# Kernel optimization log

Measured on AMD Instinct MI355X. Metric: run time of the kernel, lower is better.

Reference implementation:

```python
import jax, jax.numpy as jnp
import numpy as np

B, DP, N = 8, 3, 2048
DM, K = 128, 20
C4 = DM // 4


def _gather(pts, idx):
    # pts: (b, n, c), idx: (b, n, k) -> (b, n, k, c)
    return jax.vmap(lambda p, i: p[i])(pts, idx)


def _bn(x, gamma, beta, eps=1e-5):
    # train-mode BatchNorm1d; x: (b, c, n), stats over (batch, points)
    mu = jnp.mean(x, axis=(0, 2), keepdims=True)
    var = jnp.var(x, axis=(0, 2), keepdims=True)
    return gamma[None, :, None] * (x - mu) * jax.lax.rsqrt(var + eps) + beta[None, :, None]


def setup_inputs() -> dict:
    key = jax.random.key(0)
    ks = iter(jax.random.split(key, 32))

    def U(shape):
        s = 1.0 / np.sqrt(shape[-1])
        return jax.random.uniform(next(ks), shape, jnp.float32, -s, s)

    d = {}
    d['features'] = jax.random.normal(next(ks), (B, DP, N), jnp.float32)
    d['fc1_w'] = U((DM, DP)); d['fc1_b'] = U((DM,))
    d['fc2_w'] = U((DM, DM)); d['fc2_b'] = U((DM,))
    d['bn_g'] = jnp.ones((DM,), jnp.float32); d['bn_b'] = jnp.zeros((DM,), jnp.float32)
    d['fb1_w'] = U((DM, 2 * DP)); d['fb1_b'] = U((DM,))
    d['fb2_w'] = U((DM, DM)); d['fb2_b'] = U((DM,))
    d['fg1_w'] = U((DM, DM)); d['fg1_b'] = U((DM,))
    d['fg2_w'] = U((DM, DM)); d['fg2_b'] = U((DM,))
    d['wq'] = U((DM, DM)); d['wk'] = U((DM, DM)); d['wv'] = U((DM, DM))
    d['sa_qk_w'] = U((C4, DM))  # q_conv and k_conv share this weight
    d['sa_v_w'] = U((DM, DM)); d['sa_v_b'] = U((DM,))
    d['sa_t_w'] = U((DM, DM)); d['sa_t_b'] = U((DM,))
    d['sa_bn_g'] = jnp.ones((DM,), jnp.float32); d['sa_bn_b'] = jnp.zeros((DM,), jnp.float32)
    return d


def reference(features, fc1_w, fc1_b, fc2_w, fc2_b, bn_g, bn_b,
              fb1_w, fb1_b, fb2_w, fb2_b, fg1_w, fg1_b, fg2_w, fg2_b,
              wq, wk, wv, sa_qk_w, sa_v_w, sa_v_b, sa_t_w, sa_t_b,
              sa_bn_g, sa_bn_b):
    x = features  # (b, dp, n)
    # --- kNN: negative squared pairwise distance, top-k largest = nearest ---
    inner = -2.0 * jnp.einsum('bdn,bdm->bnm', x, x)
    xx = jnp.sum(x * x, axis=1)  # (b, n)
    pd = -xx[:, :, None] - inner - xx[:, None, :]  # (b, n, n)
    idx = jax.lax.top_k(pd, K)[1]  # (b, n, K) neighbor indices
    # --- get_graph_feature: gather neighbors, concat (nbr - ctr, ctr) ---
    xt = jnp.transpose(x, (0, 2, 1))  # (b, n, dp)
    nbr = _gather(xt, idx)  # (b, n, K, dp)
    ctr = jnp.broadcast_to(xt[:, :, None, :], nbr.shape)
    kf = jnp.concatenate([nbr - ctr, ctr], axis=-1)  # (b, n, K, 2*dp)
    # fb edge MLP
    kf = jax.nn.relu(kf @ fb1_w.T + fb1_b) @ fb2_w.T + fb2_b  # (b, n, K, DM)
    # --- point-transformer attention ---
    x1 = xt @ fc1_w.T + fc1_b  # (b, n, DM)
    q = x1 @ wq.T
    kg = _gather(x1 @ wk.T, idx)  # (b, n, K, DM)
    vg = _gather(x1 @ wv.T, idx)  # (b, n, K, DM)
    a = q[:, :, None, :] - kg + kf
    a = jax.nn.relu(a @ fg1_w.T + fg1_b) @ fg2_w.T + fg2_b  # fc_gamma
    attn = jax.nn.log_softmax(a / jnp.sqrt(jnp.float32(DM)), axis=-2)  # over K
    res = jnp.einsum('bnkf,bnkf->bnf', attn, vg + kf)  # (b, n, DM)
    res = jnp.transpose(res @ fc2_w.T + fc2_b, (0, 2, 1))  # (b, DM, n)
    res = jax.nn.relu(_bn(res, bn_g, bn_b)) + jnp.transpose(x1, (0, 2, 1))
    # --- SA_Layer: offset self-attention (q and k share weights) ---
    xqk = jnp.einsum('cd,bdn->bcn', sa_qk_w, res)  # (b, C4, n)
    energy = jnp.einsum('bcn,bcm->bnm', xqk, xqk)  # (b, n, n)
    att = jax.nn.softmax(energy, axis=-1)
    att = att / (1e-9 + jnp.sum(att, axis=1, keepdims=True))
    xv = jnp.einsum('cd,bdn->bcn', sa_v_w, res) + sa_v_b[None, :, None]
    xr = jnp.einsum('bcn,bnm->bcm', xv, att)  # x_v @ attention
    xr = jnp.einsum('cd,bdn->bcn', sa_t_w, res - xr) + sa_t_b[None, :, None]
    xr = jax.nn.relu(_bn(xr, sa_bn_g, sa_bn_b))
    out = res + xr  # (b, DM, n)
    return (jnp.transpose(out, (0, 2, 1)), attn)
```

## Files before the change

### kernel.cpp

```cpp
#include <hip/hip_runtime.h>

#define NPTS 16384
#define NB 2048
#define KNN 20

typedef __attribute__((ext_vector_type(4))) float f32x4;
typedef __attribute__((ext_vector_type(8))) short short8;

union U4S8 { uint4 q; short8 s; };
union W4   { unsigned u[4]; short8 s; };

__device__ __forceinline__ unsigned bf16_rne(float v){
    unsigned u = __float_as_uint(v);
    return (u + 0x7fffu + ((u>>16)&1u)) >> 16;
}
__device__ __forceinline__ unsigned pack_hl(float v){
    unsigned hi = bf16_rne(v);
    float r = v - __uint_as_float(hi<<16);
    unsigned lo = bf16_rne(r);
    return hi | (lo<<16);
}
__device__ __forceinline__ void split_hl(uint4 w0, uint4 w1, short8& hi, short8& lo){
    W4 h, l;
    h.u[0] = __builtin_amdgcn_perm(w0.y, w0.x, 0x05040100u);
    l.u[0] = __builtin_amdgcn_perm(w0.y, w0.x, 0x07060302u);
    h.u[1] = __builtin_amdgcn_perm(w0.w, w0.z, 0x05040100u);
    l.u[1] = __builtin_amdgcn_perm(w0.w, w0.z, 0x07060302u);
    h.u[2] = __builtin_amdgcn_perm(w1.y, w1.x, 0x05040100u);
    l.u[2] = __builtin_amdgcn_perm(w1.y, w1.x, 0x07060302u);
    h.u[3] = __builtin_amdgcn_perm(w1.w, w1.z, 0x05040100u);
    l.u[3] = __builtin_amdgcn_perm(w1.w, w1.z, 0x07060302u);
    hi = h.s; lo = l.s;
}
__device__ __forceinline__ f32x4 e3_mfma(short8 Ah, short8 Al, short8 Bh, short8 Bl){
    f32x4 acc = (f32x4){0.f,0.f,0.f,0.f};
    acc = __builtin_amdgcn_mfma_f32_16x16x32_bf16(Al, Bh, acc, 0,0,0);
    acc = __builtin_amdgcn_mfma_f32_16x16x32_bf16(Ah, Bl, acc, 0,0,0);
    acc = __builtin_amdgcn_mfma_f32_16x16x32_bf16(Ah, Bh, acc, 0,0,0);
    return acc;
}

__global__ void transpose_kernel(const float* in, float* out, int C){
    int gid = blockIdx.x*256 + threadIdx.x;
    if (gid >= 128*C) return;
    int j = gid / C, c = gid - j*C;
    out[gid] = in[c*128 + j];
}

__global__ void pack_bfrag_kernel(const float* w0, const float* w1, const float* w2, unsigned short* out){
    int gid = blockIdx.x*256 + threadIdx.x;
    if (gid >= 3*16384) return;
    int m = gid >> 14, r = gid & 16383;
    const float* W = (m==0)?w0:(m==1)?w1:w2;
    int e = r & 7, lane = (r>>3) & 63, ks = (r>>9)&3, ct = r>>11;
    int c = ct*16 + (lane&15), j = ks*32 + (lane>>4)*8 + e;
    out[gid] = (unsigned short)bf16_rne(W[c*128 + j]);
}

__global__ __launch_bounds__(256) void knn_kernel(const float* feat, int* g_idx){
    __shared__ float sx[2048], sy[2048], sz[2048];
    __shared__ int swin[32*20];
    int tid = threadIdx.x;
    int p0 = blockIdx.x * 32;
    int b = p0 >> 11;
    const float* fb = feat + b*3*2048;
    for (int i = tid; i < 2048; i += 256){ sx[i]=fb[i]; sy[i]=fb[2048+i]; sz[i]=fb[4096+i]; }
    __syncthreads();

    int chunk = tid & 7, pl = tid >> 3;
    int n = (p0 + pl) & 2047;
    double xi = sx[n], yi = sy[n], zi = sz[n];

    const double SENT = __longlong_as_double(0x7FE0000000000000ll);
    double val[20];
#pragma unroll
    for (int k=0;k<20;k++) val[k] = SENT;

    int base = chunk*256;
    for (int ii=0; ii<256; ii++){
        int i = (ii + (chunk<<2)) & 255;
        int j = base + i;
        double dx = (double)sx[j]-xi, dy = (double)sy[j]-yi, dz = (double)sz[j]-zi;
        double d2 = dx*dx + dy*dy + dz*dz;
        long long kb = ((__double_as_longlong(d2) & ~2047ll) | (long long)j) + (1ll<<61);
        double key = __longlong_as_double(kb);
#pragma unroll
        for (int s=19; s>=1; s--)
            val[s] = fmax(val[s-1], fmin(val[s], key));
        val[0] = fmin(val[0], key);
    }

    for (int kk=0; kk<20; kk++){
        double h = val[0];
        h = fmin(h, __shfl_xor(h, 1));
        h = fmin(h, __shfl_xor(h, 2));
        h = fmin(h, __shfl_xor(h, 4));
        if (val[0] == h){
            swin[pl*20 + kk] = (int)(__double_as_longlong(h) & 2047ll);
#pragma unroll
            for (int s=0;s<19;s++) val[s] = val[s+1];
            val[19] = SENT;
        }
    }
    __syncthreads();
    for (int t = tid; t < 640; t += 256)
        g_idx[p0*20 + t] = swin[t];
}

__global__ void x1_kernel(const float* feat, const float* w, const float* bias, float* x1){
    int gid = blockIdx.x*256 + threadIdx.x;
    int p = gid >> 7, c = gid & 127;
    int b = p >> 11, n = p & 2047;
    const float* fb = feat + b*6144 + n;
    float v = bias[c];
    v += w[c*3+0]*fb[0];
    v += w[c*3+1]*fb[2048];
    v += w[c*3+2]*fb[4096];
    x1[gid] = v;
}

__global__ __launch_bounds__(256) void qkv_kernel(const float* x1, const float* wqT, const float* wkT,
                                                  const float* wvT, float* q, float* k1, float* v1){
    __shared__ float sx[16][128];
    int tid = threadIdx.x;
    int p0 = blockIdx.x * 16;
    for (int t = tid; t < 2048; t += 256) sx[t>>7][t&127] = x1[p0*128 + t];
    __syncthreads();
    int cg = tid & 31, pg = tid >> 5, c0 = cg*4;
    float aq[2][4] = {{0,0,0,0},{0,0,0,0}};
    float ak[2][4] = {{0,0,0,0},{0,0,0,0}};
    float av[2][4] = {{0,0,0,0},{0,0,0,0}};
    for (int j=0;j<128;j++){
        float xa = sx[pg][j], xb = sx[pg+8][j];
        float4 wq4 = *(const float4*)&wqT[j*128 + c0];
        float4 wk4 = *(const float4*)&wkT[j*128 + c0];
        float4 wv4 = *(const float4*)&wvT[j*128 + c0];
        const float* wqp = &wq4.x; const float* wkp = &wk4.x; const float* wvp = &wv4.x;
#pragma unroll
        for (int ci=0; ci<4; ci++){
            aq[0][ci] += wqp[ci]*xa; aq[1][ci] += wqp[ci]*xb;
            ak[0][ci] += wkp[ci]*xa; ak[1][ci] += wkp[ci]*xb;
            av[0][ci] += wvp[ci]*xa; av[1][ci] += wvp[ci]*xb;
        }
    }
#pragma unroll
    for (int pp=0; pp<2; pp++){
        int p = p0 + pg + pp*8;
        *(float4*)&q [p*128 + c0] = make_float4(aq[pp][0],aq[pp][1],aq[pp][2],aq[pp][3]);
        *(float4*)&k1[p*128 + c0] = make_float4(ak[pp][0],ak[pp][1],ak[pp][2],ak[pp][3]);
        *(float4*)&v1[p*128 + c0] = make_float4(av[pp][0],av[pp][1],av[pp][2],av[pp][3]);
    }
}

__device__ __forceinline__ void stage_gemm(const unsigned* buf, const unsigned short* wb,
                                           int lane, int ct0, f32x4 acc[5][2]){
    short8 bf[2][4];
#pragma unroll
    for (int ci=0; ci<2; ci++)
#pragma unroll
    for (int ks=0; ks<4; ks++){
        U4S8 u; u.q = *(const uint4*)(wb + ((ct0+ci)*4 + ks)*512 + lane*8);
        bf[ci][ks] = u.s;
    }
#pragma unroll
    for (int rt=0; rt<5; rt++)
#pragma unroll
    for (int ci=0; ci<2; ci++)
        acc[rt][ci] = (f32x4){0.f,0.f,0.f,0.f};
    int abase = (lane&15)*132 + (lane>>4)*8;
#pragma unroll
    for (int rt=0; rt<5; rt++){
#pragma unroll
        for (int ks=0; ks<4; ks++){
            const unsigned* ap = buf + rt*16*132 + ks*32 + abase;
            uint4 w0 = *(const uint4*)ap;
            uint4 w1 = *(const uint4*)(ap+4);
            short8 hi, lo;
            split_hl(w0, w1, hi, lo);
#pragma unroll
            for (int ci=0; ci<2; ci++){
                acc[rt][ci] = __builtin_amdgcn_mfma_f32_16x16x32_bf16(hi, bf[ci][ks], acc[rt][ci], 0,0,0);
                acc[rt][ci] = __builtin_amdgcn_mfma_f32_16x16x32_bf16(lo, bf[ci][ks], acc[rt][ci], 0,0,0);
            }
        }
    }
}

__global__ __launch_bounds__(256, 3) void attn_kernel(
        const float* feat, const int* g_idx, const float* g_q, const float* g_k1, const float* g_v1,
        const unsigned short* wpk,
        const float* fb1w, const float* fb1b, const float* fb2b, const float* fg1b, const float* fg2b,
        float* g_attn, float* g_res){
    __shared__ __align__(16) unsigned buf[80*132];
    __shared__ float sh_q[512];
    __shared__ float sh_e[80*6];
    __shared__ int   sh_ix[80];
    int tid = threadIdx.x;
    int lane = tid & 63, wave = tid >> 6;
    int gp0 = blockIdx.x * 4;
    int b = gp0 >> 11;
    size_t kvbase = (size_t)b*2048*128;

    sh_q[tid]     = g_q[gp0*128 + tid];
    sh_q[tid+256] = g_q[gp0*128 + tid + 256];
    if (tid < 80){
        int r = tid;
        int nb = g_idx[gp0*20 + r];
        sh_ix[r] = nb;
        int p = (r*205) >> 12;
        int n = (gp0 & 2047) + p;
        const float* fbp = feat + b*6144;
        float cx = fbp[n], cy = fbp[2048+n], cz = fbp[4096+n];
        float nx = fbp[nb], ny = fbp[2048+nb], nz = fbp[4096+nb];
        sh_e[r*6+0] = nx-cx; sh_e[r*6+1] = ny-cy; sh_e[r*6+2] = nz-cz;
        sh_e[r*6+3] = cx;    sh_e[r*6+4] = cy;    sh_e[r*6+5] = cz;
    }
    __syncthreads();

    {
        int c = tid & 127, rh = tid >> 7;
        float w0=fb1w[c*6+0], w1=fb1w[c*6+1], w2=fb1w[c*6+2], w3=fb1w[c*6+3], w4=fb1w[c*6+4], w5=fb1w[c*6+5];
        float bb = fb1b[c];
#pragma unroll
        for (int rr=0; rr<40; rr++){
            int r = rr*2 + rh;
            const float* e = &sh_e[r*6];
            float v = bb + w0*e[0]+w1*e[1]+w2*e[2]+w3*e[3]+w4*e[4]+w5*e[5];
            buf[r*132 + c] = pack_hl(fmaxf(v, 0.f));
        }
    }
    __syncthreads();

    int ct0 = wave*2;
    int colA = ct0*16 + (lane&15);
    int colB = colA + 16;
    int quad = lane >> 4;
    f32x4 acc[5][2];

    stage_gemm(buf, wpk, lane, ct0, acc);
    {
        float bA = fb2b[colA], bB = fb2b[colB];
#pragma unroll
        for (int rt=0; rt<5; rt++)
#pragma unroll
        for (int ci=0; ci<2; ci++){
            int col = ci ? colB : colA;
            float bias = ci ? bB : bA;
#pragma unroll
            for (int reg=0; reg<4; reg++){
                int row = rt*16 + quad*4 + reg;
                float kf = acc[rt][ci][reg] + bias;
                g_attn[(size_t)(gp0*20 + row)*128 + col] = kf;
                int p = (row*205)>>12;
                int nb = sh_ix[row];
                float kg = g_k1[kvbase + (size_t)nb*128 + col];
                float ain = sh_q[p*128 + col] - kg + kf;
                acc[rt][ci][reg] = __uint_as_float(pack_hl(ain));
            }
        }
    }
    __syncthreads();
#pragma unroll
    for (int rt=0; rt<5; rt++)
#pragma unroll
    for (int ci=0; ci<2; ci++)
#pragma unroll
    for (int reg=0; reg<4; reg++){
        int row = rt*16 + quad*4 + reg;
        int col = ci ? colB : colA;
        buf[row*132 + col] = __float_as_uint(acc[rt][ci][reg]);
    }
    __syncthreads();

    stage_gemm(buf, wpk + 16384, lane, ct0, acc);
    {
        float bA = fg1b[colA], bB = fg1b[colB];
#pragma unroll
        for (int rt=0; rt<5; rt++)
#pragma unroll
        for (int ci=0; ci<2; ci++){
            float bias = ci ? bB : bA;
#pragma unroll
            for (int reg=0; reg<4; reg++)
                acc[rt][ci][reg] = __uint_as_float(pack_hl(fmaxf(acc[rt][ci][reg] + bias, 0.f)));
        }
    }
    __syncthreads();
#pragma unroll
    for (int rt=0; rt<5; rt++)
#pragma unroll
    for (int ci=0; ci<2; ci++)
#pragma unroll
    for (int reg=0; reg<4; reg++){
        int row = rt*16 + quad*4 + reg;
        int col = ci ? colB : colA;
        buf[row*132 + col] = __float_as_uint(acc[rt][ci][reg]);
    }
    __syncthreads();

    stage_gemm(buf, wpk + 32768, lane, ct0, acc);
    {
        float bA = fg2b[colA], bB = fg2b[colB];
#pragma unroll
        for (int rt=0; rt<5; rt++)
#pragma unroll
        for (int ci=0; ci<2; ci++){
            float bias = ci ? bB : bA;
#pragma unroll
            for (int reg=0; reg<4; reg++)
                acc[rt][ci][reg] += bias;
        }
    }
    __syncthreads();
#pragma unroll
    for (int rt=0; rt<5; rt++)
#pragma unroll
    for (int ci=0; ci<2; ci++)
#pragma unroll
    for (int reg=0; reg<4; reg++){
        int row = rt*16 + quad*4 + reg;
        int col = ci ? colB : colA;
        buf[row*132 + col] = __float_as_uint(acc[rt][ci][reg]);
    }
    __syncthreads();

#pragma unroll
    for (int w=0; w<2; w++){
        int wk = tid + 256*w;
        int p = wk >> 7, c = wk & 127;
        float s[20];
        float m = -3e38f;
#pragma unroll
        for (int k=0;k<20;k++){
            s[k] = __uint_as_float(buf[(p*20+k)*132 + c]) * 0.08838834764831845f;
            m = fmaxf(m, s[k]);
        }
        float sum = 0.f;
#pragma unroll
        for (int k=0;k<20;k++) sum += expf(s[k] - m);
        float L = m + logf(sum);
        float* op = g_attn + (size_t)(gp0+p)*20*128 + c;
        float res = 0.f;
#pragma unroll
        for (int k=0;k<20;k++){
            float at = s[k] - L;
            float kf = op[k*128];
            int nb = sh_ix[p*20+k];
            float vv = g_v1[kvbase + (size_t)nb*128 + c];
            res += at * (vv + kf);
            op[k*128] = at;
        }
        g_res[(gp0+p)*128 + c] = res;
    }
}

__global__ __launch_bounds__(256) void lin_kernel(const float* X, const float* WT, const float* bias, float* Y){
    __shared__ float sx[16][128];
    int tid = threadIdx.x;
    int p0 = blockIdx.x * 16;
    for (int t = tid; t < 2048; t += 256) sx[t>>7][t&127] = X[p0*128 + t];
    __syncthreads();
    int cg = tid & 31, pg = tid >> 5, c0 = cg*4;
    float a[2][4] = {{0,0,0,0},{0,0,0,0}};
    for (int j=0;j<128;j++){
        float xa = sx[pg][j], xb = sx[pg+8][j];
        float4 w4 = *(const float4*)&WT[j*128 + c0];
        const float* wp = &w4.x;
#pragma unroll
        for (int ci=0;ci<4;ci++){ a[0][ci] += wp[ci]*xa; a[1][ci] += wp[ci]*xb; }
    }
    float4 bv = *(const float4*)&bias[c0];
    const float* bp = &bv.x;
#pragma unroll
    for (int pp=0;pp<2;pp++){
        int p = p0 + pg + pp*8;
        *(float4*)&Y[p*128+c0] = make_float4(a[pp][0]+bp[0], a[pp][1]+bp[1], a[pp][2]+bp[2], a[pp][3]+bp[3]);
    }
}

__global__ __launch_bounds__(256) void l6_kernel(const float* Xa, const float* Xb, const float* WT,
                                                 const float* bias, float* Y){
    __shared__ float sx[16][128];
    int tid = threadIdx.x;
    int p0 = blockIdx.x * 16;
    for (int t = tid; t < 2048; t += 256) sx[t>>7][t&127] = Xa[p0*128 + t] - Xb[p0*128 + t];
    __syncthreads();
    int cg = tid & 31, pg = tid >> 5, c0 = cg*4;
    float a[2][4] = {{0,0,0,0},{0,0,0,0}};
    for (int j=0;j<128;j++){
        float xa = sx[pg][j], xb = sx[pg+8][j];
        float4 w4 = *(const float4*)&WT[j*128 + c0];
        const float* wp = &w4.x;
#pragma unroll
        for (int ci=0;ci<4;ci++){ a[0][ci] += wp[ci]*xa; a[1][ci] += wp[ci]*xb; }
    }
    float4 bv = *(const float4*)&bias[c0];
    const float* bp = &bv.x;
#pragma unroll
    for (int pp=0;pp<2;pp++){
        int p = p0 + pg + pp*8;
        *(float4*)&Y[p*128+c0] = make_float4(a[pp][0]+bp[0], a[pp][1]+bp[1], a[pp][2]+bp[2], a[pp][3]+bp[3]);
    }
}

__global__ __launch_bounds__(256) void l5_kernel(const float* X, const float* WvT, const float* vb,
                                                 const float* WqkT, unsigned* xvt_pk, unsigned* xqk_pk){
    __shared__ float sx[16][128];
    int tid = threadIdx.x;
    int p0 = blockIdx.x * 16;
    for (int t = tid; t < 2048; t += 256) sx[t>>7][t&127] = X[p0*128 + t];
    __syncthreads();
    int cg = tid & 31, pg = tid >> 5, c0 = cg*4;
    {
        float a[2][4] = {{0,0,0,0},{0,0,0,0}};
        for (int j=0;j<128;j++){
            float xa = sx[pg][j], xb = sx[pg+8][j];
            float4 w4 = *(const float4*)&WvT[j*128 + c0];
            const float* wp = &w4.x;
#pragma unroll
            for (int ci=0;ci<4;ci++){ a[0][ci] += wp[ci]*xa; a[1][ci] += wp[ci]*xb; }
        }
        float4 bv = *(const float4*)&vb[c0];
        const float* bp = &bv.x;
#pragma unroll
        for (int pp=0;pp<2;pp++){
            int p = p0 + pg + pp*8;
            int bb = p >> 11, n = p & 2047;
            unsigned* dst = xvt_pk + ((size_t)(bb*64 + (n>>5)))*4096 + (n&31);
#pragma unroll
            for (int ci=0;ci<4;ci++) dst[(c0+ci)*32] = pack_hl(a[pp][ci] + bp[ci]);
        }
    }
    if (cg < 8){
        int cq = cg*4;
        float a[2][4] = {{0,0,0,0},{0,0,0,0}};
        for (int j=0;j<128;j++){
            float xa = sx[pg][j], xb = sx[pg+8][j];
            float4 w4 = *(const float4*)&WqkT[j*32 + cq];
            const float* wp = &w4.x;
#pragma unroll
            for (int ci=0;ci<4;ci++){ a[0][ci] += wp[ci]*xa; a[1][ci] += wp[ci]*xb; }
        }
#pragma unroll
        for (int pp=0;pp<2;pp++){
            int p = p0 + pg + pp*8;
            uint4 w;
            w.x = pack_hl(a[pp][0]); w.y = pack_hl(a[pp][1]);
            w.z = pack_hl(a[pp][2]); w.w = pack_hl(a[pp][3]);
            *(uint4*)&xqk_pk[p*32 + cq] = w;
        }
    }
}

__global__ void bn_stats_kernel(const float* X, float* sums){
    int tid = threadIdx.x;
    int c = tid & 127, half = tid >> 7;
    int r0 = blockIdx.x*128 + half*64;
    float s = 0.f, sq = 0.f;
    for (int r = r0; r < r0+64; r++){
        float v = X[r*128 + c];
        s += v; sq += v*v;
    }
    atomicAdd(&sums[c], s);
    atomicAdd(&sums[128+c], sq);
}

__global__ void bn1_apply_kernel(const float* res2, const float* x1, const float* sums,
                                 const float* g, const float* beta, float* sres){
    int gid = blockIdx.x*256 + threadIdx.x;
    int c = gid & 127;
    float mu = sums[c] * (1.0f/16384.f);
    float var = sums[128+c] * (1.0f/16384.f) - mu*mu;
    float inv = 1.0f / sqrtf(var + 1e-5f);
    float y = g[c]*(res2[gid]-mu)*inv + beta[c];
    sres[gid] = fmaxf(y, 0.f) + x1[gid];
}

__global__ void final_kernel(const float* sres, const float* xr2, const float* sums,
                             const float* g, const float* beta, float* out0){
    int gid = blockIdx.x*256 + threadIdx.x;
    int c = gid & 127;
    float mu = sums[c] * (1.0f/16384.f);
    float var = sums[128+c] * (1.0f/16384.f) - mu*mu;
    float inv = 1.0f / sqrtf(var + 1e-5f);
    float y = g[c]*(xr2[gid]-mu)*inv + beta[c];
    out0[gid] = sres[gid] + fmaxf(y, 0.f);
}

__global__ __launch_bounds__(256) void sa_stats_kernel(const unsigned* xqk_pk, float* rm, float* irs){
    int tid = threadIdx.x;
    int lane = tid & 63, wave = tid >> 6;
    int b = blockIdx.x >> 5;
    int i0 = (blockIdx.x & 31) * 64 + wave*16;
    const unsigned* qb = xqk_pk + (size_t)b*2048*32;
    int quad = lane >> 4, l15 = lane & 15;
    const unsigned* ap = qb + (i0 + l15)*32 + quad*8;
    uint4 a0 = *(const uint4*)ap, a1 = *(const uint4*)(ap+4);
    short8 Ah, Al; split_hl(a0, a1, Ah, Al);

    float m[4] = {-3e38f,-3e38f,-3e38f,-3e38f};
    for (int jt=0; jt<128; jt++){
        const unsigned* bp = qb + (jt*16 + l15)*32 + quad*8;
        uint4 b0 = *(const uint4*)bp, b1 = *(const uint4*)(bp+4);
        short8 Bh, Bl; split_hl(b0,b1,Bh,Bl);
        f32x4 e = (f32x4){0.f,0.f,0.f,0.f};
        e = __builtin_amdgcn_mfma_f32_16x16x32_bf16(Ah, Bh, e, 0,0,0);
#pragma unroll
        for (int r=0;r<4;r++) m[r] = fmaxf(m[r], e[r]);
    }
#pragma unroll
    for (int mk=1; mk<16; mk<<=1)
#pragma unroll
        for (int r=0;r<4;r++) m[r] = fmaxf(m[r], __shfl_xor(m[r], mk));

    float s[4] = {0.f,0.f,0.f,0.f};
    for (int jt=0; jt<128; jt++){
        const unsigned* bp = qb + (jt*16 + l15)*32 + quad*8;
        uint4 b0 = *(const uint4*)bp, b1 = *(const uint4*)(bp+4);
        short8 Bh, Bl; split_hl(b0,b1,Bh,Bl);
        f32x4 e = e3_mfma(Ah,Al,Bh,Bl);
#pragma unroll
        for (int r=0;r<4;r++) s[r] += expf(e[r]-m[r]);
    }
#pragma unroll
    for (int mk=1; mk<16; mk<<=1)
#pragma unroll
        for (int r=0;r<4;r++) s[r] += __shfl_xor(s[r], mk);
    if (l15 == 0){
#pragma unroll
        for (int r=0;r<4;r++){
            int row = i0 + quad*4 + r;
            rm[b*2048+row]  = m[r];
            irs[b*2048+row] = 1.0f/s[r];
        }
    }
}

#define SXV_STR 36
#define ATT_STR 36
__global__ __launch_bounds__(256) void sa_xr_kernel(const unsigned* xqk_pk, const unsigned* xvt_pk,
                                                    const float* rm, const float* irs, float* xr){
    __shared__ __align__(16) unsigned sxv[128*SXV_STR];
    __shared__ __align__(16) unsigned attT[32*ATT_STR];
    __shared__ float scs[2][2][16];
    __shared__ float scs2[32];
    int tid = threadIdx.x;
    int lane = tid & 63, wave = tid >> 6;
    int quad = lane >> 4, l15 = lane & 15;
    int b = blockIdx.x >> 6, mt = blockIdx.x & 63;
    int m0 = mt*32;
    int rt = wave >> 1, ct = wave & 1;
    const unsigned* qb = xqk_pk + (size_t)b*2048*32;

    short8 Bmh, Bml;
    {
        const unsigned* bp = qb + (m0 + ct*16 + l15)*32 + quad*8;
        uint4 b0 = *(const uint4*)bp, b1 = *(const uint4*)(bp+4);
        split_hl(b0,b1,Bmh,Bml);
    }
    f32x4 acc[4];
#pragma unroll
    for (int cc=0;cc<4;cc++) acc[cc] = (f32x4){0.f,0.f,0.f,0.f};
    float cs_acc = 0.f;

    for (int chunk=0; chunk<64; chunk++){
        int n0 = chunk*32;
        __syncthreads();
        const unsigned* src = xvt_pk + ((size_t)(b*64 + chunk))*4096;
#pragma unroll
        for (int it=0; it<4; it++){
            int u = tid + it*256;
            int c = u >> 3, part = u & 7;
            *(uint4*)&sxv[c*SXV_STR + part*4] = *(const uint4*)(src + u*4);
        }
        const unsigned* ap = qb + (n0 + rt*16 + l15)*32 + quad*8;
        uint4 a0 = *(const uint4*)ap, a1 = *(const uint4*)(ap+4);
        short8 Ah, Al; split_hl(a0,a1,Ah,Al);
        f32x4 e = e3_mfma(Ah,Al,Bmh,Bml);
#pragma unroll
        for (int r=0;r<4;r++){
            int rowg = b*2048 + n0 + rt*16 + quad*4 + r;
            float att = expf(e[r] - rm[rowg]) * irs[rowg];
            cs_acc += att;
            attT[(ct*16+l15)*ATT_STR + rt*16 + quad*4 + r] = pack_hl(att);
        }
        __syncthreads();
        const unsigned* arp = attT + (ct*16+l15)*ATT_STR + quad*8;
        uint4 aa0 = *(const uint4*)arp, aa1 = *(const uint4*)(arp+4);
        short8 Aph, Apl; split_hl(aa0,aa1,Aph,Apl);
#pragma unroll
        for (int cc=0; cc<4; cc++){
            int c0 = (rt*4 + cc)*16;
            const unsigned* xp = &sxv[(c0 + l15)*SXV_STR + quad*8];
            uint4 x0 = *(const uint4*)xp, x1 = *(const uint4*)(xp+4);
            short8 Xh, Xl; split_hl(x0,x1,Xh,Xl);
            acc[cc] = __builtin_amdgcn_mfma_f32_16x16x32_bf16(Apl, Xh, acc[cc], 0,0,0);
            acc[cc] = __builtin_amdgcn_mfma_f32_16x16x32_bf16(Aph, Xl, acc[cc], 0,0,0);
            acc[cc] = __builtin_amdgcn_mfma_f32_16x16x32_bf16(Aph, Xh, acc[cc], 0,0,0);
        }
    }
    cs_acc += __shfl_xor(cs_acc, 16);
    cs_acc += __shfl_xor(cs_acc, 32);
    if (lane < 16) scs[ct][rt][lane] = cs_acc;
    __syncthreads();
    if (tid < 32) scs2[tid] = 1.0f / (1e-9f + scs[tid>>4][0][tid&15] + scs[tid>>4][1][tid&15]);
    __syncthreads();
#pragma unroll
    for (int cc=0; cc<4; cc++){
        int c0 = (rt*4 + cc)*16;
#pragma unroll
        for (int r=0;r<4;r++){
            int mloc = ct*16 + quad*4 + r;
            xr[(size_t)(b*2048 + m0 + mloc)*128 + c0 + l15] = acc[cc][r] * scs2[mloc];
        }
    }
}

extern "C" void kernel_launch(void* const* d_in, const int* in_sizes, int n_in,
                              void* d_out, int out_size, void* d_ws, size_t ws_size,
                              hipStream_t stream){
    (void)in_sizes; (void)n_in; (void)out_size; (void)ws_size;
    const float* feat = (const float*)d_in[0];
    const float* fc1w = (const float*)d_in[1];  const float* fc1b = (const float*)d_in[2];
    const float* fc2w = (const float*)d_in[3];  const float* fc2b = (const float*)d_in[4];
    const float* bng  = (const float*)d_in[5];  const float* bnb  = (const float*)d_in[6];
    const float* fb1w = (const float*)d_in[7];  const float* fb1b = (const float*)d_in[8];
    const float* fb2w = (const float*)d_in[9];  const float* fb2b = (const float*)d_in[10];
    const float* fg1w = (const float*)d_in[11]; const float* fg1b = (const float*)d_in[12];
    const float* fg2w = (const float*)d_in[13]; const float* fg2b = (const float*)d_in[14];
    const float* wq   = (const float*)d_in[15]; const float* wk   = (const float*)d_in[16];
    const float* wv   = (const float*)d_in[17];
    const float* saqk = (const float*)d_in[18];
    const float* savw = (const float*)d_in[19]; const float* savb = (const float*)d_in[20];
    const float* satw = (const float*)d_in[21]; const float* satb = (const float*)d_in[22];
    const float* sabng= (const float*)d_in[23]; const float* sabnb= (const float*)d_in[24];

    float* out0 = (float*)d_out;
    float* out1 = out0 + 2097152;

    char* ws = (char*)d_ws;
    size_t off = 0;
    auto A = [&](size_t bytes)->char*{
        char* r = ws + off;
        off = (off + bytes + 255) & ~(size_t)255;
        return r;
    };
    const size_t PBUF = (size_t)NPTS*128*4;
    int*      g_idx  = (int*)A((size_t)NPTS*KNN*4);
    float*    g_x1   = (float*)A(PBUF);
    float*    g_q    = (float*)A(PBUF);
    float*    g_k1   = (float*)A(PBUF);
    float*    g_v1   = (float*)A(PBUF);
    float*    g_res  = (float*)A(PBUF);
    float*    g_res2 = (float*)A(PBUF);
    float*    g_sres = (float*)A(PBUF);
    float*    g_xr   = (float*)A(PBUF);
    float*    g_xr2  = (float*)A(PBUF);
    unsigned* g_xvt_pk = (unsigned*)A((size_t)NPTS*128*4);
    unsigned* g_xqk_pk = (unsigned*)A((size_t)NPTS*32*4);
    float*    g_rm   = (float*)A((size_t)NPTS*4);
    float*    g_rs   = (float*)A((size_t)NPTS*4);
    float*    g_stats= (float*)A((size_t)512*4);
    unsigned short* g_wpk = (unsigned short*)A((size_t)3*16384*2);
    float*    g_wqT  = (float*)A(65536);
    float*    g_wkT  = (float*)A(65536);
    float*    g_wvT  = (float*)A(65536);
    float*    g_fc2T = (float*)A(65536);
    float*    g_savT = (float*)A(65536);
    float*    g_satT = (float*)A(65536);
    float*    g_sqkT = (float*)A(16384);

    float* bn1s = g_stats;
    float* bn2s = g_stats + 256;

    hipMemsetAsync(g_stats, 0, (size_t)512*4, stream);

    pack_bfrag_kernel<<<192, 256, 0, stream>>>(fb2w, fg1w, fg2w, g_wpk);
    transpose_kernel<<<64, 256, 0, stream>>>(wq,   g_wqT, 128);
    transpose_kernel<<<64, 256, 0, stream>>>(wk,   g_wkT, 128);
    transpose_kernel<<<64, 256, 0, stream>>>(wv,   g_wvT, 128);
    transpose_kernel<<<64, 256, 0, stream>>>(fc2w, g_fc2T, 128);
    transpose_kernel<<<64, 256, 0, stream>>>(savw, g_savT, 128);
    transpose_kernel<<<64, 256, 0, stream>>>(satw, g_satT, 128);
    transpose_kernel<<<16, 256, 0, stream>>>(saqk, g_sqkT, 32);

    knn_kernel<<<512, 256, 0, stream>>>(feat, g_idx);
    x1_kernel<<<8192, 256, 0, stream>>>(feat, fc1w, fc1b, g_x1);
    qkv_kernel<<<1024, 256, 0, stream>>>(g_x1, g_wqT, g_wkT, g_wvT, g_q, g_k1, g_v1);
    attn_kernel<<<4096, 256, 0, stream>>>(feat, g_idx, g_q, g_k1, g_v1, g_wpk,
                                          fb1w, fb1b, fb2b, fg1b, fg2b, out1, g_res);
    lin_kernel<<<1024, 256, 0, stream>>>(g_res, g_fc2T, fc2b, g_res2);
    bn_stats_kernel<<<128, 256, 0, stream>>>(g_res2, bn1s);
    bn1_apply_kernel<<<8192, 256, 0, stream>>>(g_res2, g_x1, bn1s, bng, bnb, g_sres);
    l5_kernel<<<1024, 256, 0, stream>>>(g_sres, g_savT, savb, g_sqkT, g_xvt_pk, g_xqk_pk);
    sa_stats_kernel<<<256, 256, 0, stream>>>(g_xqk_pk, g_rm, g_rs);
    sa_xr_kernel<<<512, 256, 0, stream>>>(g_xqk_pk, g_xvt_pk, g_rm, g_rs, g_xr);
    l6_kernel<<<1024, 256, 0, stream>>>(g_sres, g_xr, g_satT, satb, g_xr2);
    bn_stats_kernel<<<128, 256, 0, stream>>>(g_xr2, bn2s);
    final_kernel<<<8192, 256, 0, stream>>>(g_sres, g_xr2, bn2s, sabng, sabnb, out0);
}
```

Before: 858.9 us.

## Split SA attention-times-V reduction over four key chunks and prefetch tiles

The self-attention xr kernel now splits the 2048-point reduction dimension into four partitions, launching four times as many blocks, each writing partial sums and partial column sums to scratch buffers. A new combine kernel then adds the partials and applies the column normalisation. Register prefetch of the next xv tile is added so the global load overlaps with compute. This aims to fix low occupancy (512 blocks on a large GPU), at the cost of extra partial-buffer traffic, an extra launch, and reuse of the g_q and g_res2 buffers as scratch.

New measurement: 933.2 us. 1.09x slower.

```diff
diff --git a/kernel.cpp b/kernel.cpp
--- a/kernel.cpp
+++ b/kernel.cpp
@@ -538,16 +538,20 @@
 
 #define SXV_STR 36
 #define ATT_STR 36
-__global__ __launch_bounds__(256) void sa_xr_kernel(const unsigned* xqk_pk, const unsigned* xvt_pk,
-                                                    const float* rm, const float* irs, float* xr){
+#define NSPLIT 4
+__global__ __launch_bounds__(256) void sa_xr_part_kernel(const unsigned* xqk_pk, const unsigned* xvt_pk,
+                                                         const float* rm, const float* irs,
+                                                         float* part, float* cspart){
     __shared__ __align__(16) unsigned sxv[128*SXV_STR];
     __shared__ __align__(16) unsigned attT[32*ATT_STR];
     __shared__ float scs[2][2][16];
-    __shared__ float scs2[32];
     int tid = threadIdx.x;
     int lane = tid & 63, wave = tid >> 6;
     int quad = lane >> 4, l15 = lane & 15;
-    int b = blockIdx.x >> 6, mt = blockIdx.x & 63;
+    int blk = blockIdx.x;
+    int mt = blk & 63;
+    int b  = (blk >> 6) & 7;
+    int ns = blk >> 9;
     int m0 = mt*32;
     int rt = wave >> 1, ct = wave & 1;
     const unsigned* qb = xqk_pk + (size_t)b*2048*32;
@@ -563,15 +567,27 @@
     for (int cc=0;cc<4;cc++) acc[cc] = (f32x4){0.f,0.f,0.f,0.f};
     float cs_acc = 0.f;
 
-    for (int chunk=0; chunk<64; chunk++){
+    int ch0 = ns*16;
+    uint4 pre[4];
+    {
+        const unsigned* src = xvt_pk + ((size_t)(b*64 + ch0))*4096;
+#pragma unroll
+        for (int it=0; it<4; it++) pre[it] = *(const uint4*)(src + (tid + it*256)*4);
+    }
+
+    for (int ci16=0; ci16<16; ci16++){
+        int chunk = ch0 + ci16;
         int n0 = chunk*32;
         __syncthreads();
-        const unsigned* src = xvt_pk + ((size_t)(b*64 + chunk))*4096;
 #pragma unroll
         for (int it=0; it<4; it++){
             int u = tid + it*256;
-            int c = u >> 3, part = u & 7;
-            *(uint4*)&sxv[c*SXV_STR + part*4] = *(const uint4*)(src + u*4);
+            *(uint4*)&sxv[(u>>3)*SXV_STR + (u&7)*4] = pre[it];
+        }
+        if (ci16 < 15){
+            const unsigned* src = xvt_pk + ((size_t)(b*64 + chunk + 1))*4096;
+#pragma unroll
+            for (int it=0; it<4; it++) pre[it] = *(const uint4*)(src + (tid + it*256)*4);
         }
         const unsigned* ap = qb + (n0 + rt*16 + l15)*32 + quad*8;
         uint4 a0 = *(const uint4*)ap, a1 = *(const uint4*)(ap+4);
@@ -603,17 +619,25 @@
     cs_acc += __shfl_xor(cs_acc, 32);
     if (lane < 16) scs[ct][rt][lane] = cs_acc;
     __syncthreads();
-    if (tid < 32) scs2[tid] = 1.0f / (1e-9f + scs[tid>>4][0][tid&15] + scs[tid>>4][1][tid&15]);
-    __syncthreads();
+    if (tid < 32)
+        cspart[(size_t)(ns*8 + b)*2048 + m0 + tid] = scs[tid>>4][0][tid&15] + scs[tid>>4][1][tid&15];
 #pragma unroll
     for (int cc=0; cc<4; cc++){
         int c0 = (rt*4 + cc)*16;
 #pragma unroll
         for (int r=0;r<4;r++){
             int mloc = ct*16 + quad*4 + r;
-            xr[(size_t)(b*2048 + m0 + mloc)*128 + c0 + l15] = acc[cc][r] * scs2[mloc];
-        }
-    }
+            part[((size_t)(ns*8 + b)*2048 + m0 + mloc)*128 + c0 + l15] = acc[cc][r];
+        }
+    }
+}
+
+__global__ void sa_combine_kernel(const float* part, const float* cspart, float* xr){
+    int gid = blockIdx.x*256 + threadIdx.x;
+    int bm = gid >> 7;
+    float cs = cspart[bm] + cspart[bm+16384] + cspart[bm+2*16384] + cspart[bm+3*16384];
+    float v  = part[gid] + part[gid+2097152] + part[gid+2*2097152] + part[gid+3*2097152];
+    xr[gid] = v * (1.0f/(1e-9f + cs));
 }
 
 extern "C" void kernel_launch(void* const* d_in, const int* in_sizes, int n_in,
@@ -673,6 +697,9 @@
     float* bn1s = g_stats;
     float* bn2s = g_stats + 256;
 
+    float* g_part   = g_q;
+    float* g_cspart = g_res2;
+
     hipMemsetAsync(g_stats, 0, (size_t)512*4, stream);
 
     pack_bfrag_kernel<<<192, 256, 0, stream>>>(fb2w, fg1w, fg2w, g_wpk);
@@ -694,7 +721,8 @@
     bn1_apply_kernel<<<8192, 256, 0, stream>>>(g_res2, g_x1, bn1s, bng, bnb, g_sres);
     l5_kernel<<<1024, 256, 0, stream>>>(g_sres, g_savT, savb, g_sqkT, g_xvt_pk, g_xqk_pk);
     sa_stats_kernel<<<256, 256, 0, stream>>>(g_xqk_pk, g_rm, g_rs);
-    sa_xr_kernel<<<512, 256, 0, stream>>>(g_xqk_pk, g_xvt_pk, g_rm, g_rs, g_xr);
+    sa_xr_part_kernel<<<512*NSPLIT, 256, 0, stream>>>(g_xqk_pk, g_xvt_pk, g_rm, g_rs, g_part, g_cspart);
+    sa_combine_kernel<<<8192, 256, 0, stream>>>(g_part, g_cspart, g_xr);
     l6_kernel<<<1024, 256, 0, stream>>>(g_sres, g_xr, g_satT, satb, g_xr2);
     bn_stats_kernel<<<128, 256, 0, stream>>>(g_xr2, bn2s);
     final_kernel<<<8192, 256, 0, stream>>>(g_sres, g_xr2, bn2s, sabng, sabnb, out0);
```
